# Performance work log

Hardware: AMD Instinct MI355X
Metric: run time of the kernel (lower is better)

The kernel has to match this reference:

```python
import jax, jax.numpy as jnp
import numpy as np

DIM = 512
HEADS = 8
DIM_HEAD = 64
INNER = HEADS * DIM_HEAD
SCALE = DIM_HEAD ** -0.5
EPS = 1e-5


def setup_inputs() -> dict:
    key = jax.random.key(0)
    ks = jax.random.split(key, 7)
    B, N = 8, 1024
    x = jax.random.normal(ks[0], (B, N, DIM), dtype=jnp.float32)
    ORquery = jax.random.normal(ks[1], (B, N, DIM), dtype=jnp.float32)
    alpha = jax.random.uniform(ks[2], (B, N, N), dtype=jnp.float32)
    # learned params (Linear layers without bias; stored as [in, out])
    w_qkv = jax.random.normal(ks[3], (DIM, INNER * 3), dtype=jnp.float32) * (DIM ** -0.5)
    w_orq = jax.random.normal(ks[4], (DIM, INNER), dtype=jnp.float32) * (DIM ** -0.5)
    w_out = jax.random.normal(ks[5], (INNER, DIM), dtype=jnp.float32) * (INNER ** -0.5)
    ln_w = jnp.ones((DIM,), dtype=jnp.float32)
    ln_b = jnp.zeros((DIM,), dtype=jnp.float32)
    return {"x": x, "ORquery": ORquery, "alpha": alpha, "ln_w": ln_w,
            "ln_b": ln_b, "w_qkv": w_qkv, "w_orq": w_orq, "w_out": w_out}


def _layernorm(x, w, b):
    mu = jnp.mean(x, axis=-1, keepdims=True)
    var = jnp.mean(jnp.square(x - mu), axis=-1, keepdims=True)
    return (x - mu) * jax.lax.rsqrt(var + EPS) * w + b


def _split_heads(t):  # [B, N, H*D] -> [B, H, N, D]
    B, N, _ = t.shape
    return t.reshape(B, N, HEADS, DIM_HEAD).transpose(0, 2, 1, 3)


def _merge_heads(t):  # [B, H, N, D] -> [B, N, H*D]
    B, H, N, D = t.shape
    return t.transpose(0, 2, 1, 3).reshape(B, N, H * D)


def reference(x, ORquery, alpha, ln_w, ln_b, w_qkv, w_orq, w_out):
    xn = _layernorm(x, ln_w, ln_b)
    qkv = xn @ w_qkv  # [B, N, 3*INNER]
    q, k, v = jnp.split(qkv, 3, axis=-1)
    q, k, v = _split_heads(q), _split_heads(k), _split_heads(v)

    # standard attention pass
    dots = jnp.einsum('bhid,bhjd->bhij', q, k) * SCALE
    attn = jax.nn.softmax(dots, axis=-1)
    out = _merge_heads(jnp.einsum('bhij,bhjd->bhid', attn, v))

    # OR-query pass: shared K/V, diagonal logits zeroed, (1-alpha^T) rescale
    orq = _split_heads(_layernorm(ORquery, ln_w, ln_b) @ w_orq)
    ordots = jnp.einsum('bhid,bhjd->bhij', orq, k) * SCALE
    N = ordots.shape[-1]
    eye = jnp.eye(N, dtype=bool)
    ordots = jnp.where(eye, 0.0, ordots)
    ordots = ordots * (1.0 - alpha.transpose(0, 2, 1)[:, None, :, :])
    orattn = jax.nn.softmax(ordots, axis=-1)
    orout = _merge_heads(jnp.einsum('bhij,bhjd->bhid', orattn, v))

    return (out @ w_out, orout @ w_out)
```

## Files before the change

kernel.cpp:

```cpp
#include <hip/hip_runtime.h>
#include <hip/hip_fp16.h>
#include <cstdint>
#include <cstddef>

typedef unsigned short u16;
typedef unsigned int u32;
typedef __attribute__((ext_vector_type(8))) short short8;
typedef __attribute__((ext_vector_type(4))) float f32x4;

static __device__ __forceinline__ u16 f2bf(float x) {
    u32 u = __builtin_bit_cast(u32, x);
    u += 0x7FFFu + ((u >> 16) & 1u);
    return (u16)(u >> 16);
}

static __device__ __forceinline__ void gload16(const void* g, void* l) {
    __builtin_amdgcn_global_load_lds(
        (const __attribute__((address_space(1))) u32*)g,
        (__attribute__((address_space(3))) u32*)l, 16, 0, 0);
}

#define SW(row, cb) (((row) * 64) + ((((cb) ^ ((row) & 7))) * 8))

#define C_L2E 0.18033688011112042f

__global__ __launch_bounds__(256) void wtrans_kernel(
    const float* __restrict__ src, u16* __restrict__ dst, int R, int C)
{
    __shared__ float t[32][33];
    int c0 = blockIdx.x * 32, r0 = blockIdx.y * 32;
    int tx = threadIdx.x & 31, ty = threadIdx.x >> 5;
    #pragma unroll
    for (int rr = 0; rr < 32; rr += 8)
        t[ty + rr][tx] = src[(size_t)(r0 + ty + rr) * C + c0 + tx];
    __syncthreads();
    #pragma unroll
    for (int rr = 0; rr < 32; rr += 8)
        dst[(size_t)(c0 + ty + rr) * R + r0 + tx] = f2bf(t[tx][ty + rr]);
}

__global__ __launch_bounds__(256) void atrans_kernel(
    const float* __restrict__ a, u16* __restrict__ at)
{
    __shared__ float t[32][33];
    int b = blockIdx.z;
    int i0 = blockIdx.y * 32, j0 = blockIdx.x * 32;
    int tx = threadIdx.x & 31, ty = threadIdx.x >> 5;
    const float* ab = a + ((size_t)b << 20);
    u16* atb = at + ((size_t)b << 20);
    #pragma unroll
    for (int rr = 0; rr < 32; rr += 8)
        t[ty + rr][tx] = ab[(size_t)(j0 + ty + rr) * 1024 + i0 + tx];
    __syncthreads();
    #pragma unroll
    for (int rr = 0; rr < 32; rr += 8) {
        float v = C_L2E * (1.0f - t[tx][ty + rr]);
        __half hv = __float2half_rn(v);
        atb[(size_t)(i0 + ty + rr) * 1024 + j0 + tx] = __builtin_bit_cast(u16, hv);
    }
}

__global__ __launch_bounds__(256) void ln_kernel(
    const float* __restrict__ x, const float* __restrict__ orqy,
    const float* __restrict__ lw, const float* __restrict__ lb,
    u16* __restrict__ xn, u16* __restrict__ orqn)
{
    int row = blockIdx.x * 4 + (threadIdx.x >> 6);
    const float* src;
    u16* dst;
    if (row < 8192) { src = x + (size_t)row * 512; dst = xn + (size_t)row * 512; }
    else { src = orqy + (size_t)(row - 8192) * 512; dst = orqn + (size_t)(row - 8192) * 512; }
    int lane = threadIdx.x & 63;
    float4 a = *(const float4*)(src + lane * 8);
    float4 b = *(const float4*)(src + lane * 8 + 4);
    float s = a.x + a.y + a.z + a.w + b.x + b.y + b.z + b.w;
    float q = a.x*a.x + a.y*a.y + a.z*a.z + a.w*a.w
            + b.x*b.x + b.y*b.y + b.z*b.z + b.w*b.w;
    #pragma unroll
    for (int off = 32; off >= 1; off >>= 1) {
        s += __shfl_xor(s, off);
        q += __shfl_xor(q, off);
    }
    float mu = s * (1.0f / 512.0f);
    float var = q * (1.0f / 512.0f) - mu * mu;
    float rs = 1.0f / sqrtf(var + 1e-5f);
    float4 w0 = *(const float4*)(lw + lane * 8);
    float4 w1 = *(const float4*)(lw + lane * 8 + 4);
    float4 b0 = *(const float4*)(lb + lane * 8);
    float4 b1 = *(const float4*)(lb + lane * 8 + 4);
    union { u16 h[8]; uint4 v; } ou;
    ou.h[0] = f2bf((a.x - mu) * rs * w0.x + b0.x);
    ou.h[1] = f2bf((a.y - mu) * rs * w0.y + b0.y);
    ou.h[2] = f2bf((a.z - mu) * rs * w0.z + b0.z);
    ou.h[3] = f2bf((a.w - mu) * rs * w0.w + b0.w);
    ou.h[4] = f2bf((b.x - mu) * rs * w1.x + b1.x);
    ou.h[5] = f2bf((b.y - mu) * rs * w1.y + b1.y);
    ou.h[6] = f2bf((b.z - mu) * rs * w1.z + b1.z);
    ou.h[7] = f2bf((b.w - mu) * rs * w1.w + b1.w);
    *(uint4*)(dst + lane * 8) = ou.v;
}

__global__ __launch_bounds__(256) void gemm_kernel(
    const u16* __restrict__ A, const u16* __restrict__ Bt,
    int N, int K, int mode,
    u16* __restrict__ oq, u16* __restrict__ ok, u16* __restrict__ ov,
    float* __restrict__ of)
{
    __shared__ u16 As[8192];
    __shared__ u16 Bs[8192];
    int m0 = blockIdx.y * 128, n0 = blockIdx.x * 128;
    int tid = threadIdx.x;
    int w = tid >> 6, lane = tid & 63;
    int lo = lane & 15, hi = lane >> 4;
    int wm = (w >> 1) * 64, wn = (w & 1) * 64;

    int sr0 = tid >> 2, sr1 = sr0 + 64;
    int sc0 = ((tid & 3) ^ ((sr0 >> 1) & 3)) * 8;
    int sc1 = ((tid & 3) ^ ((sr1 >> 1) & 3)) * 8;
    const u16* aS0 = A + (size_t)(m0 + sr0) * K + sc0;
    const u16* aS1 = A + (size_t)(m0 + sr1) * K + sc1;
    const u16* bS0 = Bt + (size_t)(n0 + sr0) * K + sc0;
    const u16* bS1 = Bt + (size_t)(n0 + sr1) * K + sc1;
    int d0 = w * 512, d1 = 2048 + w * 512;

    int aoff[4], boff[4];
    #pragma unroll
    for (int f = 0; f < 4; ++f) {
        int ra = wm + f * 16 + lo, rb = wn + f * 16 + lo;
        aoff[f] = ra * 32 + ((hi ^ ((ra >> 1) & 3)) * 8);
        boff[f] = rb * 32 + ((hi ^ ((rb >> 1) & 3)) * 8);
    }

    f32x4 acc[4][4] = {};
    int nk = K >> 5;
    gload16(aS0, &As[d0]);
    gload16(aS1, &As[d1]);
    gload16(bS0, &Bs[d0]);
    gload16(bS1, &Bs[d1]);
    __syncthreads();
    for (int kt = 0; kt < nk; ++kt) {
        int cur = (kt & 1) << 12;
        if (kt + 1 < nk) {
            int ko = (kt + 1) * 32;
            int nxt = ((kt + 1) & 1) << 12;
            gload16(aS0 + ko, &As[nxt + d0]);
            gload16(aS1 + ko, &As[nxt + d1]);
            gload16(bS0 + ko, &Bs[nxt + d0]);
            gload16(bS1 + ko, &Bs[nxt + d1]);
        }
        short8 af[4], bfr[4];
        #pragma unroll
        for (int mf = 0; mf < 4; ++mf) af[mf] = *(const short8*)&As[cur + aoff[mf]];
        #pragma unroll
        for (int nf = 0; nf < 4; ++nf) bfr[nf] = *(const short8*)&Bs[cur + boff[nf]];
        #pragma unroll
        for (int mf = 0; mf < 4; ++mf)
            #pragma unroll
            for (int nf = 0; nf < 4; ++nf)
                acc[mf][nf] = __builtin_amdgcn_mfma_f32_16x16x32_bf16(af[mf], bfr[nf], acc[mf][nf], 0, 0, 0);
        __syncthreads();
    }
    #pragma unroll
    for (int mf = 0; mf < 4; ++mf) {
        #pragma unroll
        for (int nf = 0; nf < 4; ++nf) {
            #pragma unroll
            for (int r = 0; r < 4; ++r) {
                int row = m0 + wm + mf * 16 + hi * 4 + r;
                int col = n0 + wn + nf * 16 + lo;
                float val = acc[mf][nf][r];
                if (mode == 2) {
                    of[(size_t)row * N + col] = val;
                } else {
                    int bb = row >> 10, i = row & 1023;
                    int which = col >> 9;
                    int h = (col >> 6) & 7;
                    int d = col & 63;
                    if (mode == 0 && which == 0) val *= C_L2E;
                    u16 bv = f2bf(val);
                    if (mode == 0 && which == 2) {
                        ov[(((size_t)bb * 8 + h) * 64 + d) * 1024 + i] = bv;
                    } else {
                        size_t idx = (((size_t)bb * 8 + h) * 1024 + i) * 64 + d;
                        if (mode == 1) oq[idx] = bv;
                        else (which == 0 ? oq : ok)[idx] = bv;
                    }
                }
            }
        }
    }
}

__global__ __launch_bounds__(512) void attn_fused_kernel(
    const u16* __restrict__ Q, const u16* __restrict__ OQ,
    const u16* __restrict__ Kk, const u16* __restrict__ Vt,
    const u16* __restrict__ asc,
    u16* __restrict__ outS, u16* __restrict__ outO)
{
    __shared__ u16 Kbuf[2][4096];
    __shared__ u16 Vbuf[2][4096];
    __shared__ u16 Ps[8192];

    int id = blockIdx.x;
    int swz = (id & 7) * 64 + (id >> 3);
    int bh = swz >> 3, it = swz & 7;
    int b = bh >> 3, h = bh & 7;
    int i0 = it * 128;
    int tid = threadIdx.x;
    int w = tid >> 6, lane = tid & 63;
    int lo = lane & 15, hi = lane >> 4;

    const u16* Qb = Q + ((size_t)bh * 1024 + i0) * 64;
    const u16* Ob = OQ + ((size_t)bh * 1024 + i0) * 64;
    const u16* Kb = Kk + (size_t)bh * 1024 * 64;
    const u16* Vb = Vt + (size_t)bh * 64 * 1024;

    int sr = w * 8 + (lane >> 3);
    int sxc = ((lane & 7) ^ (sr & 7)) * 8;
    const u16* kS = Kb + (size_t)sr * 64 + sxc;
    const u16* vS = Vb + (size_t)sr * 1024 + sxc;
    int dA = w * 512;

    const u16* AbL = asc + ((size_t)b << 20) + ((size_t)(i0 + w * 16 + hi * 4) << 10) + lo;

    int qrow = w * 16 + lo;
    short8 qS0 = *(const short8*)&Qb[qrow * 64 + hi * 8];
    short8 qS1 = *(const short8*)&Qb[qrow * 64 + 32 + hi * 8];
    short8 qO0 = *(const short8*)&Ob[qrow * 64 + hi * 8];
    short8 qO1 = *(const short8*)&Ob[qrow * 64 + 32 + hi * 8];

    int jtd = it * 2 + (w >> 2);

    gload16(kS, &Kbuf[0][dA]);
    gload16(vS, &Vbuf[0][dA]);
    __syncthreads();

    f32x4 oS[4] = {}, oO[4] = {};
    float mS[4], lS[4], mO[4], lO[4];
    #pragma unroll
    for (int r = 0; r < 4; ++r) { mS[r] = -1e30f; lS[r] = 0.f; mO[r] = -1e30f; lO[r] = 0.f; }

    for (int jt = 0; jt < 16; ++jt) {
        int j0 = jt * 64;
        int c = jt & 1;
        const u16* Kc = Kbuf[c];
        const u16* Vc = Vbuf[c];

        u16 a_[16];
        #pragma unroll
        for (int jf = 0; jf < 4; ++jf)
            #pragma unroll
            for (int r = 0; r < 4; ++r)
                a_[jf * 4 + r] = AbL[(size_t)(r << 10) + j0 + jf * 16];

        if (jt < 15) {
            int jn = j0 + 64;
            gload16(kS + (size_t)jn * 64, &Kbuf[c ^ 1][dA]);
            gload16(vS + jn, &Vbuf[c ^ 1][dA]);
        }

        f32x4 s[4];
        #pragma unroll
        for (int jf = 0; jf < 4; ++jf) {
            short8 kf0 = *(const short8*)&Kc[SW(jf * 16 + lo, hi)];
            short8 kf1 = *(const short8*)&Kc[SW(jf * 16 + lo, 4 + hi)];
            f32x4 z = {};
            z = __builtin_amdgcn_mfma_f32_16x16x32_bf16(qS0, kf0, z, 0, 0, 0);
            z = __builtin_amdgcn_mfma_f32_16x16x32_bf16(qS1, kf1, z, 0, 0, 0);
            s[jf] = z;
        }
        {
            float mx4[4];
            #pragma unroll
            for (int r = 0; r < 4; ++r)
                mx4[r] = fmaxf(fmaxf(s[0][r], s[1][r]), fmaxf(s[2][r], s[3][r]));
            float need = fmaxf(fmaxf(mx4[0] - mS[0], mx4[1] - mS[1]),
                               fmaxf(mx4[2] - mS[2], mx4[3] - mS[3]));
            if (!__all(need <= 8.0f)) {
                #pragma unroll
                for (int r = 0; r < 4; ++r) {
                    float mx = mx4[r];
                    #pragma unroll
                    for (int msk = 8; msk >= 1; msk >>= 1) mx = fmaxf(mx, __shfl_xor(mx, msk));
                    float mn = fmaxf(mS[r], mx);
                    float scl = __builtin_amdgcn_exp2f(mS[r] - mn);
                    mS[r] = mn;
                    lS[r] *= scl;
                    #pragma unroll
                    for (int df = 0; df < 4; ++df) oS[df][r] *= scl;
                }
            }
            #pragma unroll
            for (int r = 0; r < 4; ++r)
                #pragma unroll
                for (int jf = 0; jf < 4; ++jf) {
                    float p = __builtin_amdgcn_exp2f(s[jf][r] - mS[r]);
                    s[jf][r] = p;
                    lS[r] += p;
                }
        }
        #pragma unroll
        for (int jf = 0; jf < 4; ++jf)
            #pragma unroll
            for (int r = 0; r < 4; ++r) {
                int prow = hi * 4 + r;
                Ps[w * 1024 + prow * 64 + ((jf * 16 + lo) ^ ((prow & 7) * 8))] = f2bf(s[jf][r]);
            }
        {
            short8 pa0 = *(const short8*)&Ps[w * 1024 + SW(lo, hi)];
            short8 pa1 = *(const short8*)&Ps[w * 1024 + SW(lo, 4 + hi)];
            #pragma unroll
            for (int df = 0; df < 4; ++df) {
                short8 v0 = *(const short8*)&Vc[SW(df * 16 + lo, hi)];
                short8 v1 = *(const short8*)&Vc[SW(df * 16 + lo, 4 + hi)];
                oS[df] = __builtin_amdgcn_mfma_f32_16x16x32_bf16(pa0, v0, oS[df], 0, 0, 0);
                oS[df] = __builtin_amdgcn_mfma_f32_16x16x32_bf16(pa1, v1, oS[df], 0, 0, 0);
            }
        }

        #pragma unroll
        for (int jf = 0; jf < 4; ++jf) {
            short8 kf0 = *(const short8*)&Kc[SW(jf * 16 + lo, hi)];
            short8 kf1 = *(const short8*)&Kc[SW(jf * 16 + lo, 4 + hi)];
            f32x4 z = {};
            z = __builtin_amdgcn_mfma_f32_16x16x32_bf16(qO0, kf0, z, 0, 0, 0);
            z = __builtin_amdgcn_mfma_f32_16x16x32_bf16(qO1, kf1, z, 0, 0, 0);
            s[jf] = z;
        }
        #pragma unroll
        for (int jf = 0; jf < 4; ++jf)
            #pragma unroll
            for (int r = 0; r < 4; ++r) {
                __half hv = __builtin_bit_cast(__half, a_[jf * 4 + r]);
                s[jf][r] *= __half2float(hv);
            }
        if (jt == jtd) {
            #pragma unroll
            for (int jf = 0; jf < 4; ++jf)
                #pragma unroll
                for (int r = 0; r < 4; ++r)
                    s[jf][r] = ((jf == (w & 3)) && (hi * 4 + r == lo)) ? 0.0f : s[jf][r];
        }
        {
            float mx4[4];
            #pragma unroll
            for (int r = 0; r < 4; ++r)
                mx4[r] = fmaxf(fmaxf(s[0][r], s[1][r]), fmaxf(s[2][r], s[3][r]));
            float need = fmaxf(fmaxf(mx4[0] - mO[0], mx4[1] - mO[1]),
                               fmaxf(mx4[2] - mO[2], mx4[3] - mO[3]));
            if (!__all(need <= 8.0f)) {
                #pragma unroll
                for (int r = 0; r < 4; ++r) {
                    float mx = mx4[r];
                    #pragma unroll
                    for (int msk = 8; msk >= 1; msk >>= 1) mx = fmaxf(mx, __shfl_xor(mx, msk));
                    float mn = fmaxf(mO[r], mx);
                    float scl = __builtin_amdgcn_exp2f(mO[r] - mn);
                    mO[r] = mn;
                    lO[r] *= scl;
                    #pragma unroll
                    for (int df = 0; df < 4; ++df) oO[df][r] *= scl;
                }
            }
            #pragma unroll
            for (int r = 0; r < 4; ++r)
                #pragma unroll
                for (int jf = 0; jf < 4; ++jf) {
                    float p = __builtin_amdgcn_exp2f(s[jf][r] - mO[r]);
                    s[jf][r] = p;
                    lO[r] += p;
                }
        }
        #pragma unroll
        for (int jf = 0; jf < 4; ++jf)
            #pragma unroll
            for (int r = 0; r < 4; ++r) {
                int prow = hi * 4 + r;
                Ps[w * 1024 + prow * 64 + ((jf * 16 + lo) ^ ((prow & 7) * 8))] = f2bf(s[jf][r]);
            }
        {
            short8 pa0 = *(const short8*)&Ps[w * 1024 + SW(lo, hi)];
            short8 pa1 = *(const short8*)&Ps[w * 1024 + SW(lo, 4 + hi)];
            #pragma unroll
            for (int df = 0; df < 4; ++df) {
                short8 v0 = *(const short8*)&Vc[SW(df * 16 + lo, hi)];
                short8 v1 = *(const short8*)&Vc[SW(df * 16 + lo, 4 + hi)];
                oO[df] = __builtin_amdgcn_mfma_f32_16x16x32_bf16(pa0, v0, oO[df], 0, 0, 0);
                oO[df] = __builtin_amdgcn_mfma_f32_16x16x32_bf16(pa1, v1, oO[df], 0, 0, 0);
            }
        }

        __syncthreads();
    }

    #pragma unroll
    for (int r = 0; r < 4; ++r) {
        float a = lS[r], c2 = lO[r];
        #pragma unroll
        for (int msk = 8; msk >= 1; msk >>= 1) {
            a += __shfl_xor(a, msk);
            c2 += __shfl_xor(c2, msk);
        }
        lS[r] = 1.0f / a;
        lO[r] = 1.0f / c2;
    }
    size_t obase = ((size_t)b * 1024 + i0 + w * 16 + hi * 4) * 512 + h * 64 + lo;
    #pragma unroll
    for (int df = 0; df < 4; ++df)
        #pragma unroll
        for (int r = 0; r < 4; ++r) {
            outS[obase + (size_t)r * 512 + df * 16] = f2bf(oS[df][r] * lS[r]);
            outO[obase + (size_t)r * 512 + df * 16] = f2bf(oO[df][r] * lO[r]);
        }
}

extern "C" void kernel_launch(void* const* d_in, const int* in_sizes, int n_in,
                              void* d_out, int out_size, void* d_ws, size_t ws_size,
                              hipStream_t stream)
{
    const float* x     = (const float*)d_in[0];
    const float* orqy  = (const float*)d_in[1];
    const float* alpha = (const float*)d_in[2];
    const float* ln_w  = (const float*)d_in[3];
    const float* ln_b  = (const float*)d_in[4];
    const float* w_qkv = (const float*)d_in[5];
    const float* w_orq = (const float*)d_in[6];
    const float* w_out = (const float*)d_in[7];
    float* outp = (float*)d_out;

    char* base = (char*)d_ws;
    size_t off = 0;
    auto alloc = [&](size_t bytes) -> char* {
        char* r = base + off;
        off += (bytes + 255) & ~(size_t)255;
        return r;
    };
    const size_t RC = 8192ull * 512 * 2;
    u16* xn       = (u16*)alloc(RC);
    u16* orqn     = (u16*)alloc(RC);
    u16* qb       = (u16*)alloc(RC);
    u16* kb       = (u16*)alloc(RC);
    u16* vb       = (u16*)alloc(RC);
    u16* orqb     = (u16*)alloc(RC);
    u16* attout   = (u16*)alloc(RC);
    u16* orattout = (u16*)alloc(RC);
    u16* wqkvT    = (u16*)alloc(1536ull * 512 * 2);
    u16* worqT    = (u16*)alloc(512ull * 512 * 2);
    u16* woutT    = (u16*)alloc(512ull * 512 * 2);
    u16* ascT     = (u16*)alloc(8ull * 1024 * 1024 * 2);

    wtrans_kernel<<<dim3(48, 16), 256, 0, stream>>>(w_qkv, wqkvT, 512, 1536);
    wtrans_kernel<<<dim3(16, 16), 256, 0, stream>>>(w_orq, worqT, 512, 512);
    wtrans_kernel<<<dim3(16, 16), 256, 0, stream>>>(w_out, woutT, 512, 512);
    atrans_kernel<<<dim3(32, 32, 8), 256, 0, stream>>>(alpha, ascT);
    ln_kernel<<<4096, 256, 0, stream>>>(x, orqy, ln_w, ln_b, xn, orqn);
    gemm_kernel<<<dim3(12, 64), 256, 0, stream>>>(xn, wqkvT, 1536, 512, 0, qb, kb, vb, nullptr);
    gemm_kernel<<<dim3(4, 64), 256, 0, stream>>>(orqn, worqT, 512, 512, 1, orqb, nullptr, nullptr, nullptr);
    attn_fused_kernel<<<dim3(512), 512, 0, stream>>>(qb, orqb, kb, vb, ascT, attout, orattout);
    gemm_kernel<<<dim3(4, 128), 256, 0, stream>>>(attout, woutT, 512, 512, 2, nullptr, nullptr, nullptr, outp);
}
```

Baseline: 174.3 us.

## Interleave standard and OR-query attention passes sharing K/V fragment loads

```diff
diff --git a/kernel.cpp b/kernel.cpp
--- a/kernel.cpp
+++ b/kernel.cpp
@@ -191,7 +191,7 @@
     }
 }
 
-__global__ __launch_bounds__(512) void attn_fused_kernel(
+__global__ __launch_bounds__(512, 4) void attn_fused_kernel(
     const u16* __restrict__ Q, const u16* __restrict__ OQ,
     const u16* __restrict__ Kk, const u16* __restrict__ Vt,
     const u16* __restrict__ asc,
@@ -199,7 +199,8 @@
 {
     __shared__ u16 Kbuf[2][4096];
     __shared__ u16 Vbuf[2][4096];
-    __shared__ u16 Ps[8192];
+    __shared__ u16 PsS[8192];
+    __shared__ u16 PsO[8192];
 
     int id = blockIdx.x;
     int swz = (id & 7) * 64 + (id >> 3);
@@ -259,21 +260,25 @@
             gload16(vS + jn, &Vbuf[c ^ 1][dA]);
         }
 
-        f32x4 s[4];
+        f32x4 sS[4], sO[4];
         #pragma unroll
         for (int jf = 0; jf < 4; ++jf) {
             short8 kf0 = *(const short8*)&Kc[SW(jf * 16 + lo, hi)];
             short8 kf1 = *(const short8*)&Kc[SW(jf * 16 + lo, 4 + hi)];
-            f32x4 z = {};
-            z = __builtin_amdgcn_mfma_f32_16x16x32_bf16(qS0, kf0, z, 0, 0, 0);
-            z = __builtin_amdgcn_mfma_f32_16x16x32_bf16(qS1, kf1, z, 0, 0, 0);
-            s[jf] = z;
-        }
+            f32x4 zS = {}, zO = {};
+            zS = __builtin_amdgcn_mfma_f32_16x16x32_bf16(qS0, kf0, zS, 0, 0, 0);
+            zS = __builtin_amdgcn_mfma_f32_16x16x32_bf16(qS1, kf1, zS, 0, 0, 0);
+            zO = __builtin_amdgcn_mfma_f32_16x16x32_bf16(qO0, kf0, zO, 0, 0, 0);
+            zO = __builtin_amdgcn_mfma_f32_16x16x32_bf16(qO1, kf1, zO, 0, 0, 0);
+            sS[jf] = zS;
+            sO[jf] = zO;
+        }
+
         {
             float mx4[4];
             #pragma unroll
             for (int r = 0; r < 4; ++r)
-                mx4[r] = fmaxf(fmaxf(s[0][r], s[1][r]), fmaxf(s[2][r], s[3][r]));
+                mx4[r] = fmaxf(fmaxf(sS[0][r], sS[1][r]), fmaxf(sS[2][r], sS[3][r]));
             float need = fmaxf(fmaxf(mx4[0] - mS[0], mx4[1] - mS[1]),
                                fmaxf(mx4[2] - mS[2], mx4[3] - mS[3]));
             if (!__all(need <= 8.0f)) {
@@ -294,8 +299,8 @@
             for (int r = 0; r < 4; ++r)
                 #pragma unroll
                 for (int jf = 0; jf < 4; ++jf) {
-                    float p = __builtin_amdgcn_exp2f(s[jf][r] - mS[r]);
-                    s[jf][r] = p;
+                    float p = __builtin_amdgcn_exp2f(sS[jf][r] - mS[r]);
+                    sS[jf][r] = p;
                     lS[r] += p;
                 }
         }
@@ -304,48 +309,28 @@
             #pragma unroll
             for (int r = 0; r < 4; ++r) {
                 int prow = hi * 4 + r;
-                Ps[w * 1024 + prow * 64 + ((jf * 16 + lo) ^ ((prow & 7) * 8))] = f2bf(s[jf][r]);
-            }
-        {
-            short8 pa0 = *(const short8*)&Ps[w * 1024 + SW(lo, hi)];
-            short8 pa1 = *(const short8*)&Ps[w * 1024 + SW(lo, 4 + hi)];
-            #pragma unroll
-            for (int df = 0; df < 4; ++df) {
-                short8 v0 = *(const short8*)&Vc[SW(df * 16 + lo, hi)];
-                short8 v1 = *(const short8*)&Vc[SW(df * 16 + lo, 4 + hi)];
-                oS[df] = __builtin_amdgcn_mfma_f32_16x16x32_bf16(pa0, v0, oS[df], 0, 0, 0);
-                oS[df] = __builtin_amdgcn_mfma_f32_16x16x32_bf16(pa1, v1, oS[df], 0, 0, 0);
-            }
-        }
-
-        #pragma unroll
-        for (int jf = 0; jf < 4; ++jf) {
-            short8 kf0 = *(const short8*)&Kc[SW(jf * 16 + lo, hi)];
-            short8 kf1 = *(const short8*)&Kc[SW(jf * 16 + lo, 4 + hi)];
-            f32x4 z = {};
-            z = __builtin_amdgcn_mfma_f32_16x16x32_bf16(qO0, kf0, z, 0, 0, 0);
-            z = __builtin_amdgcn_mfma_f32_16x16x32_bf16(qO1, kf1, z, 0, 0, 0);
-            s[jf] = z;
-        }
+                PsS[w * 1024 + prow * 64 + ((jf * 16 + lo) ^ ((prow & 7) * 8))] = f2bf(sS[jf][r]);
+            }
+
         #pragma unroll
         for (int jf = 0; jf < 4; ++jf)
             #pragma unroll
             for (int r = 0; r < 4; ++r) {
                 __half hv = __builtin_bit_cast(__half, a_[jf * 4 + r]);
-                s[jf][r] *= __half2float(hv);
+                sO[jf][r] *= __half2float(hv);
             }
         if (jt == jtd) {
             #pragma unroll
             for (int jf = 0; jf < 4; ++jf)
                 #pragma unroll
                 for (int r = 0; r < 4; ++r)
-                    s[jf][r] = ((jf == (w & 3)) && (hi * 4 + r == lo)) ? 0.0f : s[jf][r];
+                    sO[jf][r] = ((jf == (w & 3)) && (hi * 4 + r == lo)) ? 0.0f : sO[jf][r];
         }
         {
             float mx4[4];
             #pragma unroll
             for (int r = 0; r < 4; ++r)
-                mx4[r] = fmaxf(fmaxf(s[0][r], s[1][r]), fmaxf(s[2][r], s[3][r]));
+                mx4[r] = fmaxf(fmaxf(sO[0][r], sO[1][r]), fmaxf(sO[2][r], sO[3][r]));
             float need = fmaxf(fmaxf(mx4[0] - mO[0], mx4[1] - mO[1]),
                                fmaxf(mx4[2] - mO[2], mx4[3] - mO[3]));
             if (!__all(need <= 8.0f)) {
@@ -366,8 +351,8 @@
             for (int r = 0; r < 4; ++r)
                 #pragma unroll
                 for (int jf = 0; jf < 4; ++jf) {
-                    float p = __builtin_amdgcn_exp2f(s[jf][r] - mO[r]);
-                    s[jf][r] = p;
+                    float p = __builtin_amdgcn_exp2f(sO[jf][r] - mO[r]);
+                    sO[jf][r] = p;
                     lO[r] += p;
                 }
         }
@@ -376,17 +361,22 @@
             #pragma unroll
             for (int r = 0; r < 4; ++r) {
                 int prow = hi * 4 + r;
-                Ps[w * 1024 + prow * 64 + ((jf * 16 + lo) ^ ((prow & 7) * 8))] = f2bf(s[jf][r]);
-            }
+                PsO[w * 1024 + prow * 64 + ((jf * 16 + lo) ^ ((prow & 7) * 8))] = f2bf(sO[jf][r]);
+            }
+
         {
-            short8 pa0 = *(const short8*)&Ps[w * 1024 + SW(lo, hi)];
-            short8 pa1 = *(const short8*)&Ps[w * 1024 + SW(lo, 4 + hi)];
+            short8 paS0 = *(const short8*)&PsS[w * 1024 + SW(lo, hi)];
+            short8 paS1 = *(const short8*)&PsS[w * 1024 + SW(lo, 4 + hi)];
+            short8 paO0 = *(const short8*)&PsO[w * 1024 + SW(lo, hi)];
+            short8 paO1 = *(const short8*)&PsO[w * 1024 + SW(lo, 4 + hi)];
             #pragma unroll
             for (int df = 0; df < 4; ++df) {
                 short8 v0 = *(const short8*)&Vc[SW(df * 16 + lo, hi)];
                 short8 v1 = *(const short8*)&Vc[SW(df * 16 + lo, 4 + hi)];
-                oO[df] = __builtin_amdgcn_mfma_f32_16x16x32_bf16(pa0, v0, oO[df], 0, 0, 0);
-                oO[df] = __builtin_amdgcn_mfma_f32_16x16x32_bf16(pa1, v1, oO[df], 0, 0, 0);
+                oS[df] = __builtin_amdgcn_mfma_f32_16x16x32_bf16(paS0, v0, oS[df], 0, 0, 0);
+                oS[df] = __builtin_amdgcn_mfma_f32_16x16x32_bf16(paS1, v1, oS[df], 0, 0, 0);
+                oO[df] = __builtin_amdgcn_mfma_f32_16x16x32_bf16(paO0, v0, oO[df], 0, 0, 0);
+                oO[df] = __builtin_amdgcn_mfma_f32_16x16x32_bf16(paO1, v1, oO[df], 0, 0, 0);
             }
         }
 
```

Result: slower. 317.2 us (+81.9%).
